# Kernel optimization log

Measured on AMD Instinct MI355X. Metric: run time of the kernel, lower is better.

The kernel has to match this reference:

```python
import jax, jax.numpy as jnp
import numpy as np

D_MODEL, D_HIDDEN, N_EXPERTS = 1024, 4096, 8
CAP_FACTOR, LBL_COEF, ZLOSS_COEF = 1.25, 0.01, 0.0


def setup_inputs() -> dict:
    key = jax.random.key(0)
    ks = jax.random.split(key, 4)
    B, T = 4, 2048
    x = jax.random.normal(ks[0], (B, T, D_MODEL), dtype=jnp.float32)
    # router linear
    Wr = jax.random.normal(ks[1], (D_MODEL, N_EXPERTS), jnp.float32) / np.sqrt(D_MODEL).astype(np.float32)
    br = jnp.zeros((N_EXPERTS,), jnp.float32)
    # per-expert MLP: fc1 [D->H], gelu, fc2 [H->D]
    W1 = jax.random.normal(ks[2], (N_EXPERTS, D_MODEL, D_HIDDEN), jnp.float32) / np.sqrt(D_MODEL).astype(np.float32)
    b1 = jnp.zeros((N_EXPERTS, D_HIDDEN), jnp.float32)
    W2 = jax.random.normal(ks[3], (N_EXPERTS, D_HIDDEN, D_MODEL), jnp.float32) / np.sqrt(D_HIDDEN).astype(np.float32)
    b2 = jnp.zeros((N_EXPERTS, D_MODEL), jnp.float32)
    return {"x": x, "Wr": Wr, "br": br, "W1": W1, "b1": b1, "W2": W2, "b2": b2}


def reference(x, Wr, br, W1, b1, W2, b2):
    B, T, D = x.shape
    N = B * T
    E = Wr.shape[1]
    cap = int(CAP_FACTOR * (N / E) + 1)  # static Python int

    h = x.reshape(N, D)
    # --- Top1Router ---
    logits = h @ Wr + br                              # [N, E]
    probs = jax.nn.softmax(logits, axis=-1)
    top1 = jnp.argmax(probs, axis=-1)                 # [N]
    w = jnp.take_along_axis(probs, top1[:, None], axis=1)  # [N, 1]
    assign = jax.nn.one_hot(top1, E, dtype=jnp.float32)    # constant wrt grads
    importance = probs.mean(axis=0)
    load = jax.lax.stop_gradient(assign).mean(axis=0)
    lb_loss = E * jnp.sum(importance * load)
    z_loss = jnp.mean(jax.nn.logsumexp(logits, axis=-1) ** 2)

    # --- capacity-based dispatch (first `cap` tokens per expert, token order) ---
    pos = (jnp.cumsum(assign, axis=0) * assign).sum(axis=-1).astype(jnp.int32) - 1  # [N] slot within expert
    keep = pos < cap
    slot = jnp.where(keep, pos, cap)  # dropped tokens -> overflow slot `cap`
    xe = jnp.zeros((E, cap + 1, D), x.dtype).at[top1, slot].set(h)[:, :cap]  # [E, cap, D]

    # --- per-expert MLP as grouped GEMMs ---
    he = jax.nn.gelu(jnp.einsum('ecd,edh->ech', xe, W1) + b1[:, None, :])    # [E, cap, H]
    ye = jnp.einsum('ech,ehd->ecd', he, W2) + b2[:, None, :]                 # [E, cap, D]

    # --- combine (gather back, scale by router weight, zero dropped) ---
    out = ye[top1, jnp.minimum(pos, cap - 1)] * w   # [N, D]
    out = jnp.where(keep[:, None], out, jnp.zeros((), x.dtype))
    y = out.reshape(B, T, D)
    aux = LBL_COEF * lb_loss + ZLOSS_COEF * z_loss
    return (y, aux)
```

## Files before the change

kernel.cpp:

```cpp
#include <hip/hip_runtime.h>
#include <hip/hip_bf16.h>

#define N_TOK 8192
#define DM    1024
#define DH    4096
#define NE    8
#define CAP   1281
#define CAPR  1408
#define ISTR  1536

typedef unsigned short u16;
typedef __attribute__((ext_vector_type(8))) __bf16 bf16x8;
typedef __attribute__((ext_vector_type(8))) short short8;
typedef __attribute__((ext_vector_type(4))) short s16x4;
typedef __attribute__((ext_vector_type(4))) float f4;

__device__ __forceinline__ u16 f2bf(float f){
  union { float f; unsigned u; } v; v.f = f;
  unsigned r = v.u + 0x7fffu + ((v.u >> 16) & 1u);
  return (u16)(r >> 16);
}

__device__ __forceinline__ float gelu_fast(float v){
  float u = 0.7978845608028654f * (v + 0.044715f * v * v * v);
  return v * __builtin_amdgcn_rcpf(1.0f + __expf(-2.0f * u));
}

__device__ __forceinline__ void gl2lds16(const void* g, void* l){
  __builtin_amdgcn_global_load_lds((const __attribute__((address_space(1))) void*)g,
                                   (__attribute__((address_space(3))) void*)l, 16, 0, 0);
}

__global__ __launch_bounds__(256) void tcvt_k(const float* __restrict__ in, u16* __restrict__ out,
                                              int K, int Nn){
  __shared__ float tile[64][68];
  size_t mb = (size_t)blockIdx.z * (size_t)K * (size_t)Nn;
  const float* ip = in + mb;
  u16* op = out + mb;
  int n0 = blockIdx.x*64, k0 = blockIdx.y*64;
  int t = threadIdx.x;
  int kr = t>>4, nc = (t&15)*4;
  #pragma unroll
  for (int ii=0;ii<4;ii++){
    f4 v = *(const f4*)&ip[(size_t)(k0+kr+16*ii)*Nn + n0 + nc];
    tile[kr+16*ii][nc+0] = v[0]; tile[kr+16*ii][nc+1] = v[1];
    tile[kr+16*ii][nc+2] = v[2]; tile[kr+16*ii][nc+3] = v[3];
  }
  __syncthreads();
  int nr = t>>2, kc = (t&3)*16;
  short8 o0, o1;
  #pragma unroll
  for (int c=0;c<8;c++){
    o0[c] = (short)f2bf(tile[kc+c][nr]);
    o1[c] = (short)f2bf(tile[kc+8+c][nr]);
  }
  *(short8*)&op[(size_t)(n0+nr)*K + k0 + kc] = o0;
  *(short8*)&op[(size_t)(n0+nr)*K + k0 + kc + 8] = o1;
}

__global__ __launch_bounds__(256) void router_k(const float* __restrict__ x, const float* __restrict__ Wr,
    const float* __restrict__ br, u16* __restrict__ Xb, int* __restrict__ top1,
    float* __restrict__ wgt, float* __restrict__ impSum){
  __shared__ float pSh[4][8];
  int wid = threadIdx.x >> 6, lane = threadIdx.x & 63;
  int n = blockIdx.x * 4 + wid;
  const float* xr = x + (size_t)n * DM;
  u16* xbr = Xb + (size_t)n * DM;
  float acc[8];
  #pragma unroll
  for (int e=0;e<8;e++) acc[e]=0.f;
  #pragma unroll
  for (int c=0;c<4;c++){
    int d0 = c*256 + lane*4;
    f4 xv = *(const f4*)(xr + d0);
    s16x4 xb;
    #pragma unroll
    for (int j=0;j<4;j++) xb[j] = (short)f2bf(xv[j]);
    *(s16x4*)(xbr + d0) = xb;
    #pragma unroll
    for (int j=0;j<4;j++){
      const float* wrow = Wr + (size_t)(d0+j)*NE;
      float xs = xv[j];
      #pragma unroll
      for (int e=0;e<8;e++) acc[e] = fmaf(xs, wrow[e], acc[e]);
    }
  }
  #pragma unroll
  for (int off=32; off>0; off>>=1){
    #pragma unroll
    for (int e=0;e<8;e++) acc[e] += __shfl_down(acc[e], off, 64);
  }
  if (lane==0){
    float lg[8]; float mx = -1e30f;
    #pragma unroll
    for (int e=0;e<8;e++){ lg[e] = acc[e] + br[e]; mx = fmaxf(mx, lg[e]); }
    float p[8], s=0.f;
    #pragma unroll
    for (int e=0;e<8;e++){ p[e] = expf(lg[e]-mx); s += p[e]; }
    int bt=0; float bv=lg[0];
    #pragma unroll
    for (int e=1;e<8;e++){ if (lg[e]>bv){ bv=lg[e]; bt=e; } }
    float inv = 1.f/s;
    top1[n] = bt; wgt[n] = p[bt]*inv;
    #pragma unroll
    for (int e=0;e<8;e++) pSh[wid][e] = p[e]*inv;
  }
  __syncthreads();
  if (threadIdx.x < 8){
    int e = threadIdx.x;
    atomicAdd(&impSum[e], pSh[0][e]+pSh[1][e]+pSh[2][e]+pSh[3][e]);
  }
}

__global__ __launch_bounds__(1024) void scan_k(const int* __restrict__ top1, int* __restrict__ idx,
    int* __restrict__ cnt, int* __restrict__ rawcnt, int* __restrict__ dropList,
    int* __restrict__ nDrop, const float* __restrict__ impSum, float* __restrict__ auxOut){
  __shared__ int waveCnt[16][8];
  __shared__ int wavePre[16][8];
  __shared__ int chunkTot[8];
  __shared__ int base_s[8];
  int tid = threadIdx.x, wid = tid>>6, lane = tid&63;
  if (tid < 8) base_s[tid] = 0;
  __syncthreads();
  for (int c=0;c<8;c++){
    int t = c*1024 + tid;
    int e = top1[t];
    int myPre = 0;
    #pragma unroll
    for (int ex=0; ex<8; ex++){
      unsigned long long mk = __ballot(e == ex);
      if (lane == 0) waveCnt[wid][ex] = __popcll(mk);
      if (ex == e) myPre = __popcll(mk & ((1ull<<lane)-1ull));
    }
    __syncthreads();
    if (tid < 8){
      int run = 0;
      for (int wv=0; wv<16; wv++){ wavePre[wv][tid] = run; run += waveCnt[wv][tid]; }
      chunkTot[tid] = run;
    }
    __syncthreads();
    int pos = base_s[e] + wavePre[wid][e] + myPre;
    if (pos < CAP) idx[e*ISTR + pos] = t;
    else { int d = atomicAdd(nDrop, 1); dropList[d] = t; }
    __syncthreads();
    if (tid < 8) base_s[tid] += chunkTot[tid];
    __syncthreads();
  }
  if (tid < 8){
    rawcnt[tid] = base_s[tid];
    cnt[tid] = base_s[tid] < CAP ? base_s[tid] : CAP;
  }
  if (tid == 0){
    float s = 0.f;
    for (int e=0;e<8;e++) s += (impSum[e]*(1.f/N_TOK)) * ((float)base_s[e]*(1.f/N_TOK));
    *auxOut = 0.01f * 8.f * s;
  }
}

__global__ __launch_bounds__(256) void zdrop_k(const int* __restrict__ dropList,
    const int* __restrict__ nDrop, float* __restrict__ y){
  int nd = *nDrop;
  for (int i = blockIdx.x; i < nd; i += gridDim.x){
    int t = dropList[i];
    f4* row = (f4*)(y + (size_t)t * DM);
    f4 z; z[0]=0.f; z[1]=0.f; z[2]=0.f; z[3]=0.f;
    row[threadIdx.x] = z;
  }
}


#define LDA(buf, m, kk) (*(const bf16x8*)&lds[(buf)*16384 + (aBase ^ ((kk)*32)) + (m)*1024])
#define LDB(buf, n, kk) (*(const bf16x8*)&lds[32768 + (buf)*16384 + (bBase ^ ((kk)*32)) + (n)*1024])

#define SA_J(buf, j, kc) gl2lds16(aS[j] + (size_t)(kc)*64, &lds[(buf)*16384 + ((j)*512 + t)*8])
#define SB_ALLM(buf, kc) do{ \
  gl2lds16(bS[0] + (size_t)(kc)*64, &lds[32768 + (buf)*16384 + (0*512 + t)*8]); \
  gl2lds16(bS[1] + (size_t)(kc)*64, &lds[32768 + (buf)*16384 + (1*512 + t)*8]); \
  gl2lds16(bS[2] + (size_t)(kc)*64, &lds[32768 + (buf)*16384 + (2*512 + t)*8]); \
  gl2lds16(bS[3] + (size_t)(kc)*64, &lds[32768 + (buf)*16384 + (3*512 + t)*8]); }while(0)

#define LGKM0 do{ asm volatile("s_waitcnt lgkmcnt(0)" ::: "memory"); \
                  __builtin_amdgcn_sched_barrier(0); }while(0)

#define MFMA_PAIR(q) \
  _Pragma("unroll") for (int j_=0;j_<2;j_++) \
    _Pragma("unroll") for (int n_=0;n_<4;n_++) \
      _Pragma("unroll") for (int kk_=0;kk_<2;kk_++) \
        acc[2*(q)+j_][n_] = __builtin_amdgcn_mfma_f32_16x16x32_bf16(a_[j_][kk_], Bf[n_][kk_], acc[2*(q)+j_][n_], 0,0,0);

#define KTILE(buf, ktv, NTv) do{ \
  int kc1 = (ktv)+1 < (NTv) ? (ktv)+1 : (NTv)-1; \
  int kc2 = (ktv)+2 < (NTv) ? (ktv)+2 : (NTv)-1; \
  bf16x8 a_[2][2]; \
   \
  asm volatile("s_waitcnt vmcnt(6)" ::: "memory"); \
  __builtin_amdgcn_s_barrier(); \
  _Pragma("unroll") for (int n_=0;n_<4;n_++){ Bf[n_][0] = LDB(buf,n_,0); Bf[n_][1] = LDB(buf,n_,1); } \
  a_[0][0]=LDA(buf,0,0); a_[0][1]=LDA(buf,0,1); a_[1][0]=LDA(buf,1,0); a_[1][1]=LDA(buf,1,1); \
  SA_J((buf)^1, 1, kc1); SA_J((buf)^1, 3, kc1); \
  LGKM0; \
  __builtin_amdgcn_s_setprio(1); MFMA_PAIR(0); __builtin_amdgcn_s_setprio(0); \
   \
  __builtin_amdgcn_s_barrier(); \
  a_[0][0]=LDA(buf,2,0); a_[0][1]=LDA(buf,2,1); a_[1][0]=LDA(buf,3,0); a_[1][1]=LDA(buf,3,1); \
  SB_ALLM(buf, kc2); \
  LGKM0; \
  __builtin_amdgcn_s_setprio(1); MFMA_PAIR(1); __builtin_amdgcn_s_setprio(0); \
   \
  __builtin_amdgcn_s_barrier(); \
  a_[0][0]=LDA(buf,4,0); a_[0][1]=LDA(buf,4,1); a_[1][0]=LDA(buf,5,0); a_[1][1]=LDA(buf,5,1); \
  SA_J(buf, 0, kc2); SA_J(buf, 2, kc2); \
  LGKM0; \
  __builtin_amdgcn_s_setprio(1); MFMA_PAIR(2); __builtin_amdgcn_s_setprio(0); \
   \
  __builtin_amdgcn_s_barrier(); \
  a_[0][0]=LDA(buf,6,0); a_[0][1]=LDA(buf,6,1); a_[1][0]=LDA(buf,7,0); a_[1][1]=LDA(buf,7,1); \
  LGKM0; \
  __builtin_amdgcn_s_setprio(1); MFMA_PAIR(3); __builtin_amdgcn_s_setprio(0); \
}while(0)

#define GEMM_PROLOGUE() do{ \
  SB_ALLM(0, 0); \
  SA_J(0,0,0); SA_J(0,2,0); \
  SA_J(0,1,0); SA_J(0,3,0); \
  SB_ALLM(1, 1); \
  SA_J(1,0,1); SA_J(1,2,1); }while(0)

__global__ __launch_bounds__(512, 2) void gemm1_k(
    const u16* __restrict__ Xb, const u16* __restrict__ W1T,
    const float* __restrict__ b1, const int* __restrict__ idx,
    const int* __restrict__ cnt, u16* __restrict__ He)
{
  int e = blockIdx.z, mt = blockIdx.y, nt = blockIdx.x;
  int cn = cnt[e];
  if (mt*256 >= cn) return;
  __shared__ __align__(16) u16 lds[65536];
  int t = threadIdx.x, lane = t&63, wid = t>>6;
  int waveM = wid>>2, waveN = wid&3;
  int rA = lane&15, kb = lane>>4, s = rA&7;

  const u16* aS[4]; const u16* bS[4];
  #pragma unroll
  for (int j=0;j<4;j++){
    int pos = j*512 + t;
    int row = pos>>3, ch = pos&7;
    int gcb = ch ^ (row&7);
    int slotrow = mt*256 + row;
    int token = (slotrow < cn) ? idx[e*ISTR + slotrow] : 0;
    aS[j] = Xb + (size_t)token*DM + gcb*8;
    bS[j] = W1T + ((size_t)e*DH + nt*256 + row)*DM + gcb*8;
  }
  f4 acc[8][4];
  #pragma unroll
  for (int m=0;m<8;m++)
    #pragma unroll
    for (int n=0;n<4;n++)
      #pragma unroll
      for (int j=0;j<4;j++) acc[m][n][j]=0.f;

  int aBase = (waveM*128 + rA)*64 + (kb ^ s)*8;
  int bBase = (waveN*64  + rA)*64 + (kb ^ s)*8;
  bf16x8 Bf[4][2];

  GEMM_PROLOGUE();
  const int NT = DM/64;
  #pragma unroll 1
  for (int i=0;i<NT/2;i++){
    KTILE(0, 2*i,   NT);
    KTILE(1, 2*i+1, NT);
  }
  asm volatile("s_waitcnt vmcnt(0) lgkmcnt(0)" ::: "memory");

  int rG = lane>>4;
  #pragma unroll
  for (int n=0;n<4;n++){
    int col = nt*256 + waveN*64 + n*16 + rA;
    float bias = b1[e*DH + col];
    #pragma unroll
    for (int m=0;m<8;m++){
      int slot = mt*256 + waveM*128 + m*16 + rG*4;
      if (slot < CAPR){
        u16* dst = He + ((size_t)e*CAPR + slot)*DH + col;
        #pragma unroll
        for (int j=0;j<4;j++){
          float v = acc[m][n][j] + bias;
          dst[(size_t)j*DH] = f2bf(gelu_fast(v));
        }
      }
    }
  }
}

__global__ __launch_bounds__(512, 2) void gemm2_k(
    const u16* __restrict__ He, const u16* __restrict__ W2T,
    const float* __restrict__ b2, const int* __restrict__ idx,
    const int* __restrict__ cnt, const float* __restrict__ wgt,
    float* __restrict__ y)
{
  int e = blockIdx.z, mt = blockIdx.y, nt = blockIdx.x;
  int cn = cnt[e];
  if (mt*256 >= cn) return;
  __shared__ __align__(16) u16 lds[65536];
  int t = threadIdx.x, lane = t&63, wid = t>>6;
  int waveM = wid>>2, waveN = wid&3;
  int rA = lane&15, kb = lane>>4, s = rA&7;

  const u16* aS[4]; const u16* bS[4];
  #pragma unroll
  for (int j=0;j<4;j++){
    int pos = j*512 + t;
    int row = pos>>3, ch = pos&7;
    int gcb = ch ^ (row&7);
    int srow = mt*256 + row; if (srow >= cn) srow = cn-1;
    aS[j] = He  + ((size_t)e*CAPR + srow)*DH + gcb*8;
    bS[j] = W2T + ((size_t)e*DM + nt*256 + row)*DH + gcb*8;
  }
  f4 acc[8][4];
  #pragma unroll
  for (int m=0;m<8;m++)
    #pragma unroll
    for (int n=0;n<4;n++)
      #pragma unroll
      for (int j=0;j<4;j++) acc[m][n][j]=0.f;

  int aBase = (waveM*128 + rA)*64 + (kb ^ s)*8;
  int bBase = (waveN*64  + rA)*64 + (kb ^ s)*8;
  bf16x8 Bf[4][2];

  GEMM_PROLOGUE();
  const int NT = DH/64;
  #pragma unroll 1
  for (int i=0;i<NT/2;i++){
    KTILE(0, 2*i,   NT);
    KTILE(1, 2*i+1, NT);
  }
  asm volatile("s_waitcnt vmcnt(0) lgkmcnt(0)" ::: "memory");

  int rG = lane>>4;
  float bias_[4];
  #pragma unroll
  for (int n=0;n<4;n++) bias_[n] = b2[e*DM + nt*256 + waveN*64 + n*16 + rA];
  #pragma unroll
  for (int m=0;m<8;m++){
    int slot0 = mt*256 + waveM*128 + m*16 + rG*4;
    #pragma unroll
    for (int j=0;j<4;j++){
      int slot = slot0 + j;
      bool valid = slot < cn;
      int tk = valid ? idx[e*ISTR + slot] : 0;
      float wv = valid ? wgt[tk] : 0.f;
      float* yr = y + (size_t)tk*DM;
      #pragma unroll
      for (int n=0;n<4;n++){
        int col = nt*256 + waveN*64 + n*16 + rA;
        if (valid) yr[col] = (acc[m][n][j] + bias_[n]) * wv;
      }
    }
  }
}

extern "C" void kernel_launch(void* const* d_in, const int* in_sizes, int n_in,
                              void* d_out, int out_size, void* d_ws, size_t ws_size,
                              hipStream_t stream){
  const float* x  = (const float*)d_in[0];
  const float* Wr = (const float*)d_in[1];
  const float* br = (const float*)d_in[2];
  const float* W1 = (const float*)d_in[3];
  const float* b1 = (const float*)d_in[4];
  const float* W2 = (const float*)d_in[5];
  const float* b2 = (const float*)d_in[6];
  float* y = (float*)d_out;

  char* ws = (char*)d_ws;
  u16* Xb  = (u16*)(ws);
  u16* W1T = (u16*)(ws + 16777216ull);
  u16* W2T = (u16*)(ws + 16777216ull + 67108864ull);
  u16* He  = (u16*)(ws + 16777216ull + 2ull*67108864ull);
  char* tail = ws + 16777216ull + 2ull*67108864ull + (size_t)NE*CAPR*DH*2ull;
  int*   top1 = (int*)(tail);
  float* wgt  = (float*)(tail + 32768);
  int*   idx  = (int*)(tail + 65536);
  int*   drop = (int*)(tail + 65536 + 49152);
  float* impSum = (float*)(tail + 65536 + 49152 + 32768);
  int*   nDrop  = (int*)((char*)impSum + 32);
  int*   cnt    = nDrop + 1;
  int*   rawcnt = cnt + 8;

  (void)hipMemsetAsync(impSum, 0, 64, stream);

  tcvt_k<<<dim3(64,16,8), 256, 0, stream>>>(W1, W1T, DM, DH);
  tcvt_k<<<dim3(16,64,8), 256, 0, stream>>>(W2, W2T, DH, DM);
  router_k<<<2048, 256, 0, stream>>>(x, Wr, br, Xb, top1, wgt, impSum);
  scan_k<<<1, 1024, 0, stream>>>(top1, idx, cnt, rawcnt, drop, nDrop, impSum,
                                 y + (size_t)N_TOK*DM);
  zdrop_k<<<64, 256, 0, stream>>>(drop, nDrop, y);
  gemm1_k<<<dim3(DH/256, 6, NE), 512, 0, stream>>>(Xb, W1T, b1, idx, cnt, He);
  gemm2_k<<<dim3(DM/256, 6, NE), 512, 0, stream>>>(He, W2T, b2, idx, cnt, wgt, y);

  (void)in_sizes; (void)n_in; (void)out_size; (void)ws_size;
}
```

Baseline: 356.2 us.

## Split-K the second expert GEMM, stage epilogues through LDS, add combine kernel

Splits the second expert GEMM's K dimension in two, so each half writes fp32 partial sums to a workspace buffer and the launch gets more blocks to fill the device. A new per-token combine kernel adds the two partials and the bias, applies the router weight and zeroes dropped tokens, replacing the drop-list zeroing kernel and the scattered epilogue writes. Both GEMM epilogues now stage tiles in LDS so global stores are coalesced vector writes. The first GEMM grid is cut to 5 row tiles and partials are sized for 1280 slots, so a token landing in slot 1280 (capacity 1281) would not be computed correctly. The change also adds extra traffic for the partial buffer.

```diff
diff --git a/kernel.cpp b/kernel.cpp
--- a/kernel.cpp
+++ b/kernel.cpp
@@ -8,6 +8,7 @@
 #define CAP   1281
 #define CAPR  1408
 #define ISTR  1536
+#define PR    1280
 
 typedef unsigned short u16;
 typedef __attribute__((ext_vector_type(8))) __bf16 bf16x8;
@@ -113,8 +114,8 @@
 }
 
 __global__ __launch_bounds__(1024) void scan_k(const int* __restrict__ top1, int* __restrict__ idx,
-    int* __restrict__ cnt, int* __restrict__ rawcnt, int* __restrict__ dropList,
-    int* __restrict__ nDrop, const float* __restrict__ impSum, float* __restrict__ auxOut){
+    int* __restrict__ slotOf, int* __restrict__ cnt,
+    const float* __restrict__ impSum, float* __restrict__ auxOut){
   __shared__ int waveCnt[16][8];
   __shared__ int wavePre[16][8];
   __shared__ int chunkTot[8];
@@ -140,14 +141,14 @@
     }
     __syncthreads();
     int pos = base_s[e] + wavePre[wid][e] + myPre;
-    if (pos < CAP) idx[e*ISTR + pos] = t;
-    else { int d = atomicAdd(nDrop, 1); dropList[d] = t; }
+    bool keep = pos < CAP;
+    if (keep) idx[e*ISTR + pos] = t;
+    slotOf[t] = keep ? pos : -1;
     __syncthreads();
     if (tid < 8) base_s[tid] += chunkTot[tid];
     __syncthreads();
   }
   if (tid < 8){
-    rawcnt[tid] = base_s[tid];
     cnt[tid] = base_s[tid] < CAP ? base_s[tid] : CAP;
   }
   if (tid == 0){
@@ -157,15 +158,25 @@
   }
 }
 
-__global__ __launch_bounds__(256) void zdrop_k(const int* __restrict__ dropList,
-    const int* __restrict__ nDrop, float* __restrict__ y){
-  int nd = *nDrop;
-  for (int i = blockIdx.x; i < nd; i += gridDim.x){
-    int t = dropList[i];
-    f4* row = (f4*)(y + (size_t)t * DM);
-    f4 z; z[0]=0.f; z[1]=0.f; z[2]=0.f; z[3]=0.f;
-    row[threadIdx.x] = z;
-  }
+__global__ __launch_bounds__(256) void combine_k(const float* __restrict__ part,
+    const float* __restrict__ b2, const int* __restrict__ top1,
+    const int* __restrict__ slotOf, const float* __restrict__ wgt,
+    float* __restrict__ y){
+  int t = blockIdx.x;
+  int d = threadIdx.x*4;
+  int s = slotOf[t];
+  f4 o; o[0]=0.f; o[1]=0.f; o[2]=0.f; o[3]=0.f;
+  if (s >= 0){
+    int e = top1[t];
+    float w = wgt[t];
+    size_t base = ((size_t)e*PR + s)*DM + d;
+    f4 a = *(const f4*)&part[base];
+    f4 b = *(const f4*)&part[(size_t)NE*PR*DM + base];
+    f4 c = *(const f4*)&b2[e*DM + d];
+    #pragma unroll
+    for (int i=0;i<4;i++) o[i] = (a[i]+b[i]+c[i])*w;
+  }
+  *(f4*)&y[(size_t)t*DM + d] = o;
 }
 
 
@@ -192,7 +203,6 @@
   int kc1 = (ktv)+1 < (NTv) ? (ktv)+1 : (NTv)-1; \
   int kc2 = (ktv)+2 < (NTv) ? (ktv)+2 : (NTv)-1; \
   bf16x8 a_[2][2]; \
-   \
   asm volatile("s_waitcnt vmcnt(6)" ::: "memory"); \
   __builtin_amdgcn_s_barrier(); \
   _Pragma("unroll") for (int n_=0;n_<4;n_++){ Bf[n_][0] = LDB(buf,n_,0); Bf[n_][1] = LDB(buf,n_,1); } \
@@ -200,19 +210,16 @@
   SA_J((buf)^1, 1, kc1); SA_J((buf)^1, 3, kc1); \
   LGKM0; \
   __builtin_amdgcn_s_setprio(1); MFMA_PAIR(0); __builtin_amdgcn_s_setprio(0); \
-   \
   __builtin_amdgcn_s_barrier(); \
   a_[0][0]=LDA(buf,2,0); a_[0][1]=LDA(buf,2,1); a_[1][0]=LDA(buf,3,0); a_[1][1]=LDA(buf,3,1); \
   SB_ALLM(buf, kc2); \
   LGKM0; \
   __builtin_amdgcn_s_setprio(1); MFMA_PAIR(1); __builtin_amdgcn_s_setprio(0); \
-   \
   __builtin_amdgcn_s_barrier(); \
   a_[0][0]=LDA(buf,4,0); a_[0][1]=LDA(buf,4,1); a_[1][0]=LDA(buf,5,0); a_[1][1]=LDA(buf,5,1); \
   SA_J(buf, 0, kc2); SA_J(buf, 2, kc2); \
   LGKM0; \
   __builtin_amdgcn_s_setprio(1); MFMA_PAIR(2); __builtin_amdgcn_s_setprio(0); \
-   \
   __builtin_amdgcn_s_barrier(); \
   a_[0][0]=LDA(buf,6,0); a_[0][1]=LDA(buf,6,1); a_[1][0]=LDA(buf,7,0); a_[1][1]=LDA(buf,7,1); \
   LGKM0; \
@@ -270,34 +277,40 @@
     KTILE(1, 2*i+1, NT);
   }
   asm volatile("s_waitcnt vmcnt(0) lgkmcnt(0)" ::: "memory");
+  __builtin_amdgcn_s_barrier();
 
   int rG = lane>>4;
-  #pragma unroll
-  for (int n=0;n<4;n++){
-    int col = nt*256 + waveN*64 + n*16 + rA;
-    float bias = b1[e*DH + col];
-    #pragma unroll
-    for (int m=0;m<8;m++){
-      int slot = mt*256 + waveM*128 + m*16 + rG*4;
-      if (slot < CAPR){
-        u16* dst = He + ((size_t)e*CAPR + slot)*DH + col;
-        #pragma unroll
-        for (int j=0;j<4;j++){
-          float v = acc[m][n][j] + bias;
-          dst[(size_t)j*DH] = f2bf(gelu_fast(v));
-        }
-      }
+  float bias_[4];
+  #pragma unroll
+  for (int n=0;n<4;n++) bias_[n] = b1[e*DH + nt*256 + waveN*64 + n*16 + rA];
+  u16* stg = &lds[wid*1280];
+  #pragma unroll 1
+  for (int m=0;m<8;m++){
+    #pragma unroll
+    for (int n=0;n<4;n++)
+      #pragma unroll
+      for (int j=0;j<4;j++)
+        stg[(rG*4+j)*72 + n*16 + rA] = f2bf(gelu_fast(acc[m][n][j] + bias_[n]));
+    asm volatile("s_waitcnt lgkmcnt(0)" ::: "memory");
+    __builtin_amdgcn_sched_barrier(0);
+    int slot = mt*256 + waveM*128 + m*16;
+    #pragma unroll
+    for (int h=0;h<2;h++){
+      int row16 = h*8 + (lane>>3);
+      int c8 = (lane&7)*8;
+      bf16x8 v = *(const bf16x8*)&stg[row16*72 + c8];
+      *(bf16x8*)&He[((size_t)e*CAPR + slot + row16)*DH + nt*256 + waveN*64 + c8] = v;
     }
+    asm volatile("s_waitcnt lgkmcnt(0)" ::: "memory");
+    __builtin_amdgcn_sched_barrier(0);
   }
 }
 
 __global__ __launch_bounds__(512, 2) void gemm2_k(
     const u16* __restrict__ He, const u16* __restrict__ W2T,
-    const float* __restrict__ b2, const int* __restrict__ idx,
-    const int* __restrict__ cnt, const float* __restrict__ wgt,
-    float* __restrict__ y)
+    const int* __restrict__ cnt, float* __restrict__ part)
 {
-  int e = blockIdx.z, mt = blockIdx.y, nt = blockIdx.x;
+  int e = blockIdx.z, mt = blockIdx.y >> 1, ks = blockIdx.y & 1, nt = blockIdx.x;
   int cn = cnt[e];
   if (mt*256 >= cn) return;
   __shared__ __align__(16) u16 lds[65536];
@@ -312,8 +325,8 @@
     int row = pos>>3, ch = pos&7;
     int gcb = ch ^ (row&7);
     int srow = mt*256 + row; if (srow >= cn) srow = cn-1;
-    aS[j] = He  + ((size_t)e*CAPR + srow)*DH + gcb*8;
-    bS[j] = W2T + ((size_t)e*DM + nt*256 + row)*DH + gcb*8;
+    aS[j] = He  + ((size_t)e*CAPR + srow)*DH + ks*2048 + gcb*8;
+    bS[j] = W2T + ((size_t)e*DM + nt*256 + row)*DH + ks*2048 + gcb*8;
   }
   f4 acc[8][4];
   #pragma unroll
@@ -328,34 +341,37 @@
   bf16x8 Bf[4][2];
 
   GEMM_PROLOGUE();
-  const int NT = DH/64;
+  const int NT = 2048/64;
   #pragma unroll 1
   for (int i=0;i<NT/2;i++){
     KTILE(0, 2*i,   NT);
     KTILE(1, 2*i+1, NT);
   }
   asm volatile("s_waitcnt vmcnt(0) lgkmcnt(0)" ::: "memory");
+  __builtin_amdgcn_s_barrier();
 
   int rG = lane>>4;
-  float bias_[4];
-  #pragma unroll
-  for (int n=0;n<4;n++) bias_[n] = b2[e*DM + nt*256 + waveN*64 + n*16 + rA];
-  #pragma unroll
+  float* stgf = ((float*)lds) + wid*1088;
+  float* pOut = part + ((size_t)ks*NE + e)*((size_t)PR*DM);
+  #pragma unroll 1
   for (int m=0;m<8;m++){
-    int slot0 = mt*256 + waveM*128 + m*16 + rG*4;
-    #pragma unroll
-    for (int j=0;j<4;j++){
-      int slot = slot0 + j;
-      bool valid = slot < cn;
-      int tk = valid ? idx[e*ISTR + slot] : 0;
-      float wv = valid ? wgt[tk] : 0.f;
-      float* yr = y + (size_t)tk*DM;
+    #pragma unroll
+    for (int n=0;n<4;n++)
       #pragma unroll
-      for (int n=0;n<4;n++){
-        int col = nt*256 + waveN*64 + n*16 + rA;
-        if (valid) yr[col] = (acc[m][n][j] + bias_[n]) * wv;
-      }
+      for (int j=0;j<4;j++)
+        stgf[(rG*4+j)*68 + n*16 + rA] = acc[m][n][j];
+    asm volatile("s_waitcnt lgkmcnt(0)" ::: "memory");
+    __builtin_amdgcn_sched_barrier(0);
+    int slot = mt*256 + waveM*128 + m*16;
+    #pragma unroll
+    for (int it=0; it<4; it++){
+      int row16 = it*4 + rG;
+      int wc = (lane&15)*4;
+      f4 v = *(const f4*)&stgf[row16*68 + wc];
+      *(f4*)&pOut[(size_t)(slot+row16)*DM + nt*256 + waveN*64 + wc] = v;
     }
+    asm volatile("s_waitcnt lgkmcnt(0)" ::: "memory");
+    __builtin_amdgcn_sched_barrier(0);
   }
 }
 
@@ -374,28 +390,26 @@
   char* ws = (char*)d_ws;
   u16* Xb  = (u16*)(ws);
   u16* W1T = (u16*)(ws + 16777216ull);
-  u16* W2T = (u16*)(ws + 16777216ull + 67108864ull);
-  u16* He  = (u16*)(ws + 16777216ull + 2ull*67108864ull);
-  char* tail = ws + 16777216ull + 2ull*67108864ull + (size_t)NE*CAPR*DH*2ull;
-  int*   top1 = (int*)(tail);
-  float* wgt  = (float*)(tail + 32768);
-  int*   idx  = (int*)(tail + 65536);
-  int*   drop = (int*)(tail + 65536 + 49152);
+  float* part = (float*)ws;
+  u16* W2T = (u16*)(ws + 83886080ull);
+  u16* He  = (u16*)(ws + 83886080ull + 67108864ull);
+  char* tail = ws + 83886080ull + 67108864ull + (size_t)NE*CAPR*DH*2ull;
+  int*   top1   = (int*)(tail);
+  float* wgt    = (float*)(tail + 32768);
+  int*   idx    = (int*)(tail + 65536);
+  int*   slotOf = (int*)(tail + 65536 + 49152);
   float* impSum = (float*)(tail + 65536 + 49152 + 32768);
-  int*   nDrop  = (int*)((char*)impSum + 32);
-  int*   cnt    = nDrop + 1;
-  int*   rawcnt = cnt + 8;
-
-  (void)hipMemsetAsync(impSum, 0, 64, stream);
+  int*   cnt    = (int*)((char*)impSum + 32);
+
+  (void)hipMemsetAsync(impSum, 0, 32, stream);
 
   tcvt_k<<<dim3(64,16,8), 256, 0, stream>>>(W1, W1T, DM, DH);
   tcvt_k<<<dim3(16,64,8), 256, 0, stream>>>(W2, W2T, DH, DM);
   router_k<<<2048, 256, 0, stream>>>(x, Wr, br, Xb, top1, wgt, impSum);
-  scan_k<<<1, 1024, 0, stream>>>(top1, idx, cnt, rawcnt, drop, nDrop, impSum,
-                                 y + (size_t)N_TOK*DM);
-  zdrop_k<<<64, 256, 0, stream>>>(drop, nDrop, y);
-  gemm1_k<<<dim3(DH/256, 6, NE), 512, 0, stream>>>(Xb, W1T, b1, idx, cnt, He);
-  gemm2_k<<<dim3(DM/256, 6, NE), 512, 0, stream>>>(He, W2T, b2, idx, cnt, wgt, y);
+  scan_k<<<1, 1024, 0, stream>>>(top1, idx, slotOf, cnt, impSum, y + (size_t)N_TOK*DM);
+  gemm1_k<<<dim3(DH/256, 5, NE), 512, 0, stream>>>(Xb, W1T, b1, idx, cnt, He);
+  gemm2_k<<<dim3(DM/256, 10, NE), 512, 0, stream>>>(He, W2T, cnt, part);
+  combine_k<<<N_TOK, 256, 0, stream>>>(part, b2, top1, slotOf, wgt, y);
 
   (void)in_sizes; (void)n_in; (void)out_size; (void)ws_size;
 }
```

New measurement: 476.6 us. +33.8%, slower.

## Fuse fp32-to-bf16 weight conversion into GEMM B-tile loads, drop transpose kernels

Applied to the files above, without the earlier changes.

Removes the two separate transpose-and-convert passes over W1 and W2. Each GEMM now reads fp32 weight rows straight into registers, packs them to bf16 with v_cvt_pk_bf16_f32 and writes them into swizzled LDS, using a new LDB addressing scheme and a reworked prefetch and waitcnt schedule. It also flattens the grid and maps blocks so that tiles sharing an expert and N-tile stay on the same XCD. The cost is twice the global weight bytes per GEMM tile, re-read by every M-tile, plus extra VALU conversion work inside the main loop.

```diff
diff --git a/kernel.cpp b/kernel.cpp
--- a/kernel.cpp
+++ b/kernel.cpp
@@ -14,6 +14,7 @@
 typedef __attribute__((ext_vector_type(8))) short short8;
 typedef __attribute__((ext_vector_type(4))) short s16x4;
 typedef __attribute__((ext_vector_type(4))) float f4;
+typedef __attribute__((ext_vector_type(4))) unsigned int ui32x4;
 
 __device__ __forceinline__ u16 f2bf(float f){
   union { float f; unsigned u; } v; v.f = f;
@@ -29,33 +30,6 @@
 __device__ __forceinline__ void gl2lds16(const void* g, void* l){
   __builtin_amdgcn_global_load_lds((const __attribute__((address_space(1))) void*)g,
                                    (__attribute__((address_space(3))) void*)l, 16, 0, 0);
-}
-
-__global__ __launch_bounds__(256) void tcvt_k(const float* __restrict__ in, u16* __restrict__ out,
-                                              int K, int Nn){
-  __shared__ float tile[64][68];
-  size_t mb = (size_t)blockIdx.z * (size_t)K * (size_t)Nn;
-  const float* ip = in + mb;
-  u16* op = out + mb;
-  int n0 = blockIdx.x*64, k0 = blockIdx.y*64;
-  int t = threadIdx.x;
-  int kr = t>>4, nc = (t&15)*4;
-  #pragma unroll
-  for (int ii=0;ii<4;ii++){
-    f4 v = *(const f4*)&ip[(size_t)(k0+kr+16*ii)*Nn + n0 + nc];
-    tile[kr+16*ii][nc+0] = v[0]; tile[kr+16*ii][nc+1] = v[1];
-    tile[kr+16*ii][nc+2] = v[2]; tile[kr+16*ii][nc+3] = v[3];
-  }
-  __syncthreads();
-  int nr = t>>2, kc = (t&3)*16;
-  short8 o0, o1;
-  #pragma unroll
-  for (int c=0;c<8;c++){
-    o0[c] = (short)f2bf(tile[kc+c][nr]);
-    o1[c] = (short)f2bf(tile[kc+8+c][nr]);
-  }
-  *(short8*)&op[(size_t)(n0+nr)*K + k0 + kc] = o0;
-  *(short8*)&op[(size_t)(n0+nr)*K + k0 + kc + 8] = o1;
 }
 
 __global__ __launch_bounds__(256) void router_k(const float* __restrict__ x, const float* __restrict__ Wr,
@@ -113,8 +87,8 @@
 }
 
 __global__ __launch_bounds__(1024) void scan_k(const int* __restrict__ top1, int* __restrict__ idx,
-    int* __restrict__ cnt, int* __restrict__ rawcnt, int* __restrict__ dropList,
-    int* __restrict__ nDrop, const float* __restrict__ impSum, float* __restrict__ auxOut){
+    int* __restrict__ cnt, int* __restrict__ dropList, int* __restrict__ nDrop,
+    const float* __restrict__ impSum, float* __restrict__ auxOut){
   __shared__ int waveCnt[16][8];
   __shared__ int wavePre[16][8];
   __shared__ int chunkTot[8];
@@ -147,7 +121,6 @@
     __syncthreads();
   }
   if (tid < 8){
-    rawcnt[tid] = base_s[tid];
     cnt[tid] = base_s[tid] < CAP ? base_s[tid] : CAP;
   }
   if (tid == 0){
@@ -170,14 +143,29 @@
 
 
 #define LDA(buf, m, kk) (*(const bf16x8*)&lds[(buf)*16384 + (aBase ^ ((kk)*32)) + (m)*1024])
-#define LDB(buf, n, kk) (*(const bf16x8*)&lds[32768 + (buf)*16384 + (bBase ^ ((kk)*32)) + (n)*1024])
-
-#define SA_J(buf, j, kc) gl2lds16(aS[j] + (size_t)(kc)*64, &lds[(buf)*16384 + ((j)*512 + t)*8])
-#define SB_ALLM(buf, kc) do{ \
-  gl2lds16(bS[0] + (size_t)(kc)*64, &lds[32768 + (buf)*16384 + (0*512 + t)*8]); \
-  gl2lds16(bS[1] + (size_t)(kc)*64, &lds[32768 + (buf)*16384 + (1*512 + t)*8]); \
-  gl2lds16(bS[2] + (size_t)(kc)*64, &lds[32768 + (buf)*16384 + (2*512 + t)*8]); \
-  gl2lds16(bS[3] + (size_t)(kc)*64, &lds[32768 + (buf)*16384 + (3*512 + t)*8]); }while(0)
+#define LDB(buf, n_, kk) (*(const bf16x8*)&lds[32768 + (buf)*16384 + \
+  (waveN*64 + (n_)*16 + rA)*64 + ((((kb ^ ((4*(n_) + (rA>>2)) & 7)))*8) ^ ((kk)*32))])
+
+#define SA_ALL(buf, kc) do{ \
+  gl2lds16(aS[0] + (size_t)(kc)*64, &lds[(buf)*16384 + (0*512 + t)*8]); \
+  gl2lds16(aS[1] + (size_t)(kc)*64, &lds[(buf)*16384 + (1*512 + t)*8]); \
+  gl2lds16(aS[2] + (size_t)(kc)*64, &lds[(buf)*16384 + (2*512 + t)*8]); \
+  gl2lds16(aS[3] + (size_t)(kc)*64, &lds[(buf)*16384 + (3*512 + t)*8]); }while(0)
+
+#define BLOAD(kc) do{ \
+  const float* _r = wB + (size_t)((kc)*64 + wid*8)*NW + (lane<<2); \
+  _Pragma("unroll") for (int j_=0;j_<8;j_++) br[j_] = *(const f4*)(_r + (size_t)j_*NW); }while(0)
+
+#define CVTW_B(bufsel) do{ \
+  _Pragma("unroll") for (int i_=0;i_<4;i_++){ \
+    unsigned _q0,_q1,_q2,_q3; \
+    asm volatile("v_cvt_pk_bf16_f32 %0, %1, %2" : "=v"(_q0) : "v"(br[0][i_]), "v"(br[1][i_])); \
+    asm volatile("v_cvt_pk_bf16_f32 %0, %1, %2" : "=v"(_q1) : "v"(br[2][i_]), "v"(br[3][i_])); \
+    asm volatile("v_cvt_pk_bf16_f32 %0, %1, %2" : "=v"(_q2) : "v"(br[4][i_]), "v"(br[5][i_])); \
+    asm volatile("v_cvt_pk_bf16_f32 %0, %1, %2" : "=v"(_q3) : "v"(br[6][i_]), "v"(br[7][i_])); \
+    ui32x4 _qq; _qq[0]=_q0; _qq[1]=_q1; _qq[2]=_q2; _qq[3]=_q3; \
+    *(ui32x4*)&lds[32768 + (bufsel)*16384 + 256*lane + 64*i_ + 8*(wid ^ (lane&7))] = _qq; \
+  } }while(0)
 
 #define LGKM0 do{ asm volatile("s_waitcnt lgkmcnt(0)" ::: "memory"); \
                   __builtin_amdgcn_sched_barrier(0); }while(0)
@@ -193,45 +181,51 @@
   int kc2 = (ktv)+2 < (NTv) ? (ktv)+2 : (NTv)-1; \
   bf16x8 a_[2][2]; \
    \
-  asm volatile("s_waitcnt vmcnt(6)" ::: "memory"); \
+  asm volatile("s_waitcnt vmcnt(8)" ::: "memory"); \
   __builtin_amdgcn_s_barrier(); \
   _Pragma("unroll") for (int n_=0;n_<4;n_++){ Bf[n_][0] = LDB(buf,n_,0); Bf[n_][1] = LDB(buf,n_,1); } \
   a_[0][0]=LDA(buf,0,0); a_[0][1]=LDA(buf,0,1); a_[1][0]=LDA(buf,1,0); a_[1][1]=LDA(buf,1,1); \
-  SA_J((buf)^1, 1, kc1); SA_J((buf)^1, 3, kc1); \
+  SA_ALL((buf)^1, kc1); \
   LGKM0; \
   __builtin_amdgcn_s_setprio(1); MFMA_PAIR(0); __builtin_amdgcn_s_setprio(0); \
    \
   __builtin_amdgcn_s_barrier(); \
   a_[0][0]=LDA(buf,2,0); a_[0][1]=LDA(buf,2,1); a_[1][0]=LDA(buf,3,0); a_[1][1]=LDA(buf,3,1); \
-  SB_ALLM(buf, kc2); \
   LGKM0; \
   __builtin_amdgcn_s_setprio(1); MFMA_PAIR(1); __builtin_amdgcn_s_setprio(0); \
    \
   __builtin_amdgcn_s_barrier(); \
   a_[0][0]=LDA(buf,4,0); a_[0][1]=LDA(buf,4,1); a_[1][0]=LDA(buf,5,0); a_[1][1]=LDA(buf,5,1); \
-  SA_J(buf, 0, kc2); SA_J(buf, 2, kc2); \
   LGKM0; \
   __builtin_amdgcn_s_setprio(1); MFMA_PAIR(2); __builtin_amdgcn_s_setprio(0); \
    \
   __builtin_amdgcn_s_barrier(); \
   a_[0][0]=LDA(buf,6,0); a_[0][1]=LDA(buf,6,1); a_[1][0]=LDA(buf,7,0); a_[1][1]=LDA(buf,7,1); \
+  asm volatile("s_waitcnt vmcnt(4)" ::: "memory"); \
+  CVTW_B((buf)^1); \
+  BLOAD(kc2); \
   LGKM0; \
   __builtin_amdgcn_s_setprio(1); MFMA_PAIR(3); __builtin_amdgcn_s_setprio(0); \
 }while(0)
 
 #define GEMM_PROLOGUE() do{ \
-  SB_ALLM(0, 0); \
-  SA_J(0,0,0); SA_J(0,2,0); \
-  SA_J(0,1,0); SA_J(0,3,0); \
-  SB_ALLM(1, 1); \
-  SA_J(1,0,1); SA_J(1,2,1); }while(0)
+  BLOAD(0); \
+  SA_ALL(0, 0); \
+  asm volatile("s_waitcnt vmcnt(4)" ::: "memory"); \
+  CVTW_B(0); \
+  BLOAD(1); \
+  LGKM0; }while(0)
 
 __global__ __launch_bounds__(512, 2) void gemm1_k(
-    const u16* __restrict__ Xb, const u16* __restrict__ W1T,
+    const u16* __restrict__ Xb, const float* __restrict__ W1,
     const float* __restrict__ b1, const int* __restrict__ idx,
     const int* __restrict__ cnt, u16* __restrict__ He)
 {
-  int e = blockIdx.z, mt = blockIdx.y, nt = blockIdx.x;
+  int bid = blockIdx.x;
+  int xcd = bid & 7, q = bid >> 3;
+  int gi = q / 6, mt = q - gi*6;
+  int g = gi*8 + xcd;
+  int e = g >> 4, nt = g & 15;
   int cn = cnt[e];
   if (mt*256 >= cn) return;
   __shared__ __align__(16) u16 lds[65536];
@@ -239,7 +233,7 @@
   int waveM = wid>>2, waveN = wid&3;
   int rA = lane&15, kb = lane>>4, s = rA&7;
 
-  const u16* aS[4]; const u16* bS[4];
+  const u16* aS[4];
   #pragma unroll
   for (int j=0;j<4;j++){
     int pos = j*512 + t;
@@ -248,8 +242,10 @@
     int slotrow = mt*256 + row;
     int token = (slotrow < cn) ? idx[e*ISTR + slotrow] : 0;
     aS[j] = Xb + (size_t)token*DM + gcb*8;
-    bS[j] = W1T + ((size_t)e*DH + nt*256 + row)*DM + gcb*8;
-  }
+  }
+  const float* wB = W1 + (size_t)e*DM*DH + nt*256;
+  const int NW = DH;
+  f4 br[8];
   f4 acc[8][4];
   #pragma unroll
   for (int m=0;m<8;m++)
@@ -259,7 +255,6 @@
       for (int j=0;j<4;j++) acc[m][n][j]=0.f;
 
   int aBase = (waveM*128 + rA)*64 + (kb ^ s)*8;
-  int bBase = (waveN*64  + rA)*64 + (kb ^ s)*8;
   bf16x8 Bf[4][2];
 
   GEMM_PROLOGUE();
@@ -292,12 +287,16 @@
 }
 
 __global__ __launch_bounds__(512, 2) void gemm2_k(
-    const u16* __restrict__ He, const u16* __restrict__ W2T,
+    const u16* __restrict__ He, const float* __restrict__ W2,
     const float* __restrict__ b2, const int* __restrict__ idx,
     const int* __restrict__ cnt, const float* __restrict__ wgt,
     float* __restrict__ y)
 {
-  int e = blockIdx.z, mt = blockIdx.y, nt = blockIdx.x;
+  int bid = blockIdx.x;
+  int xcd = bid & 7, q = bid >> 3;
+  int gi = q / 6, mt = q - gi*6;
+  int g = gi*8 + xcd;
+  int e = g >> 2, nt = g & 3;
   int cn = cnt[e];
   if (mt*256 >= cn) return;
   __shared__ __align__(16) u16 lds[65536];
@@ -305,16 +304,18 @@
   int waveM = wid>>2, waveN = wid&3;
   int rA = lane&15, kb = lane>>4, s = rA&7;
 
-  const u16* aS[4]; const u16* bS[4];
+  const u16* aS[4];
   #pragma unroll
   for (int j=0;j<4;j++){
     int pos = j*512 + t;
     int row = pos>>3, ch = pos&7;
     int gcb = ch ^ (row&7);
     int srow = mt*256 + row; if (srow >= cn) srow = cn-1;
-    aS[j] = He  + ((size_t)e*CAPR + srow)*DH + gcb*8;
-    bS[j] = W2T + ((size_t)e*DM + nt*256 + row)*DH + gcb*8;
-  }
+    aS[j] = He + ((size_t)e*CAPR + srow)*DH + gcb*8;
+  }
+  const float* wB = W2 + (size_t)e*DH*DM + nt*256;
+  const int NW = DM;
+  f4 br[8];
   f4 acc[8][4];
   #pragma unroll
   for (int m=0;m<8;m++)
@@ -324,7 +325,6 @@
       for (int j=0;j<4;j++) acc[m][n][j]=0.f;
 
   int aBase = (waveM*128 + rA)*64 + (kb ^ s)*8;
-  int bBase = (waveN*64  + rA)*64 + (kb ^ s)*8;
   bf16x8 Bf[4][2];
 
   GEMM_PROLOGUE();
@@ -373,29 +373,24 @@
 
   char* ws = (char*)d_ws;
   u16* Xb  = (u16*)(ws);
-  u16* W1T = (u16*)(ws + 16777216ull);
-  u16* W2T = (u16*)(ws + 16777216ull + 67108864ull);
-  u16* He  = (u16*)(ws + 16777216ull + 2ull*67108864ull);
-  char* tail = ws + 16777216ull + 2ull*67108864ull + (size_t)NE*CAPR*DH*2ull;
-  int*   top1 = (int*)(tail);
-  float* wgt  = (float*)(tail + 32768);
-  int*   idx  = (int*)(tail + 65536);
-  int*   drop = (int*)(tail + 65536 + 49152);
+  u16* He  = (u16*)(ws + 16777216ull);
+  char* tail = ws + 16777216ull + (size_t)NE*CAPR*DH*2ull;
+  int*   top1   = (int*)(tail);
+  float* wgt    = (float*)(tail + 32768);
+  int*   idx    = (int*)(tail + 65536);
+  int*   drop   = (int*)(tail + 65536 + 49152);
   float* impSum = (float*)(tail + 65536 + 49152 + 32768);
   int*   nDrop  = (int*)((char*)impSum + 32);
   int*   cnt    = nDrop + 1;
-  int*   rawcnt = cnt + 8;
 
   (void)hipMemsetAsync(impSum, 0, 64, stream);
 
-  tcvt_k<<<dim3(64,16,8), 256, 0, stream>>>(W1, W1T, DM, DH);
-  tcvt_k<<<dim3(16,64,8), 256, 0, stream>>>(W2, W2T, DH, DM);
   router_k<<<2048, 256, 0, stream>>>(x, Wr, br, Xb, top1, wgt, impSum);
-  scan_k<<<1, 1024, 0, stream>>>(top1, idx, cnt, rawcnt, drop, nDrop, impSum,
+  scan_k<<<1, 1024, 0, stream>>>(top1, idx, cnt, drop, nDrop, impSum,
                                  y + (size_t)N_TOK*DM);
   zdrop_k<<<64, 256, 0, stream>>>(drop, nDrop, y);
-  gemm1_k<<<dim3(DH/256, 6, NE), 512, 0, stream>>>(Xb, W1T, b1, idx, cnt, He);
-  gemm2_k<<<dim3(DM/256, 6, NE), 512, 0, stream>>>(He, W2T, b2, idx, cnt, wgt, y);
+  gemm1_k<<<768, 512, 0, stream>>>(Xb, W1, b1, idx, cnt, He);
+  gemm2_k<<<192, 512, 0, stream>>>(He, W2, b2, idx, cnt, wgt, y);
 
   (void)in_sizes; (void)n_in; (void)out_size; (void)ws_size;
 }
```

Result: slower. 425.8 us (+19.6%).

## Swap GEMM1 operand roles, vectorize He stores, and remap blocks for XCD locality

Applied to the files above, without the earlier changes.

GEMM1 now treats W1T as the M operand and gathered tokens as the N operand, so the accumulator layout lets each lane write four contiguous bf16 hidden values with a single 8-byte store. The bias is loaded as a float4. Both GEMMs switch to a 1D grid with a block-index remap that groups tiles of the same expert and weight slice onto the same XCD, aiming for better L2 reuse. The rawcnt output is removed. One risk is that the He padding rows between cn and CAPR are no longer written, although GEMM2 clamps its reads to cn-1.

```diff
diff --git a/kernel.cpp b/kernel.cpp
--- a/kernel.cpp
+++ b/kernel.cpp
@@ -113,8 +113,8 @@
 }
 
 __global__ __launch_bounds__(1024) void scan_k(const int* __restrict__ top1, int* __restrict__ idx,
-    int* __restrict__ cnt, int* __restrict__ rawcnt, int* __restrict__ dropList,
-    int* __restrict__ nDrop, const float* __restrict__ impSum, float* __restrict__ auxOut){
+    int* __restrict__ cnt, int* __restrict__ dropList, int* __restrict__ nDrop,
+    const float* __restrict__ impSum, float* __restrict__ auxOut){
   __shared__ int waveCnt[16][8];
   __shared__ int wavePre[16][8];
   __shared__ int chunkTot[8];
@@ -147,7 +147,6 @@
     __syncthreads();
   }
   if (tid < 8){
-    rawcnt[tid] = base_s[tid];
     cnt[tid] = base_s[tid] < CAP ? base_s[tid] : CAP;
   }
   if (tid == 0){
@@ -168,7 +167,6 @@
   }
 }
 
-
 #define LDA(buf, m, kk) (*(const bf16x8*)&lds[(buf)*16384 + (aBase ^ ((kk)*32)) + (m)*1024])
 #define LDB(buf, n, kk) (*(const bf16x8*)&lds[32768 + (buf)*16384 + (bBase ^ ((kk)*32)) + (n)*1024])
 
@@ -192,7 +190,6 @@
   int kc1 = (ktv)+1 < (NTv) ? (ktv)+1 : (NTv)-1; \
   int kc2 = (ktv)+2 < (NTv) ? (ktv)+2 : (NTv)-1; \
   bf16x8 a_[2][2]; \
-   \
   asm volatile("s_waitcnt vmcnt(6)" ::: "memory"); \
   __builtin_amdgcn_s_barrier(); \
   _Pragma("unroll") for (int n_=0;n_<4;n_++){ Bf[n_][0] = LDB(buf,n_,0); Bf[n_][1] = LDB(buf,n_,1); } \
@@ -200,19 +197,16 @@
   SA_J((buf)^1, 1, kc1); SA_J((buf)^1, 3, kc1); \
   LGKM0; \
   __builtin_amdgcn_s_setprio(1); MFMA_PAIR(0); __builtin_amdgcn_s_setprio(0); \
-   \
   __builtin_amdgcn_s_barrier(); \
   a_[0][0]=LDA(buf,2,0); a_[0][1]=LDA(buf,2,1); a_[1][0]=LDA(buf,3,0); a_[1][1]=LDA(buf,3,1); \
   SB_ALLM(buf, kc2); \
   LGKM0; \
   __builtin_amdgcn_s_setprio(1); MFMA_PAIR(1); __builtin_amdgcn_s_setprio(0); \
-   \
   __builtin_amdgcn_s_barrier(); \
   a_[0][0]=LDA(buf,4,0); a_[0][1]=LDA(buf,4,1); a_[1][0]=LDA(buf,5,0); a_[1][1]=LDA(buf,5,1); \
   SA_J(buf, 0, kc2); SA_J(buf, 2, kc2); \
   LGKM0; \
   __builtin_amdgcn_s_setprio(1); MFMA_PAIR(2); __builtin_amdgcn_s_setprio(0); \
-   \
   __builtin_amdgcn_s_barrier(); \
   a_[0][0]=LDA(buf,6,0); a_[0][1]=LDA(buf,6,1); a_[1][0]=LDA(buf,7,0); a_[1][1]=LDA(buf,7,1); \
   LGKM0; \
@@ -231,9 +225,13 @@
     const float* __restrict__ b1, const int* __restrict__ idx,
     const int* __restrict__ cnt, u16* __restrict__ He)
 {
-  int e = blockIdx.z, mt = blockIdx.y, nt = blockIdx.x;
+  int bid = blockIdx.x;
+  int x = bid & 7, k = bid >> 3;
+  int g = x*16 + k/6;
+  int ntS = k - (k/6)*6;
+  int e = g >> 4, mtH = g & 15;
   int cn = cnt[e];
-  if (mt*256 >= cn) return;
+  if (ntS*256 >= cn) return;
   __shared__ __align__(16) u16 lds[65536];
   int t = threadIdx.x, lane = t&63, wid = t>>6;
   int waveM = wid>>2, waveN = wid&3;
@@ -245,10 +243,10 @@
     int pos = j*512 + t;
     int row = pos>>3, ch = pos&7;
     int gcb = ch ^ (row&7);
-    int slotrow = mt*256 + row;
+    aS[j] = W1T + ((size_t)e*DH + mtH*256 + row)*DM + gcb*8;
+    int slotrow = ntS*256 + row;
     int token = (slotrow < cn) ? idx[e*ISTR + slotrow] : 0;
-    aS[j] = Xb + (size_t)token*DM + gcb*8;
-    bS[j] = W1T + ((size_t)e*DH + nt*256 + row)*DM + gcb*8;
+    bS[j] = Xb + (size_t)token*DM + gcb*8;
   }
   f4 acc[8][4];
   #pragma unroll
@@ -273,19 +271,17 @@
 
   int rG = lane>>4;
   #pragma unroll
-  for (int n=0;n<4;n++){
-    int col = nt*256 + waveN*64 + n*16 + rA;
-    float bias = b1[e*DH + col];
-    #pragma unroll
-    for (int m=0;m<8;m++){
-      int slot = mt*256 + waveM*128 + m*16 + rG*4;
-      if (slot < CAPR){
-        u16* dst = He + ((size_t)e*CAPR + slot)*DH + col;
+  for (int m=0;m<8;m++){
+    int h0 = mtH*256 + waveM*128 + m*16 + rG*4;
+    f4 b4 = *(const f4*)&b1[e*DH + h0];
+    #pragma unroll
+    for (int n=0;n<4;n++){
+      int slot = ntS*256 + waveN*64 + n*16 + rA;
+      if (slot < cn){
+        s16x4 v;
         #pragma unroll
-        for (int j=0;j<4;j++){
-          float v = acc[m][n][j] + bias;
-          dst[(size_t)j*DH] = f2bf(gelu_fast(v));
-        }
+        for (int j=0;j<4;j++) v[j] = (short)f2bf(gelu_fast(acc[m][n][j] + b4[j]));
+        *(s16x4*)&He[((size_t)e*CAPR + slot)*DH + h0] = v;
       }
     }
   }
@@ -297,7 +293,11 @@
     const int* __restrict__ cnt, const float* __restrict__ wgt,
     float* __restrict__ y)
 {
-  int e = blockIdx.z, mt = blockIdx.y, nt = blockIdx.x;
+  int bid = blockIdx.x;
+  int x = bid & 7, k = bid >> 3;
+  int g = x*4 + k/6;
+  int mt = k - (k/6)*6;
+  int e = g >> 2, nt = g & 3;
   int cn = cnt[e];
   if (mt*256 >= cn) return;
   __shared__ __align__(16) u16 lds[65536];
@@ -377,25 +377,24 @@
   u16* W2T = (u16*)(ws + 16777216ull + 67108864ull);
   u16* He  = (u16*)(ws + 16777216ull + 2ull*67108864ull);
   char* tail = ws + 16777216ull + 2ull*67108864ull + (size_t)NE*CAPR*DH*2ull;
-  int*   top1 = (int*)(tail);
-  float* wgt  = (float*)(tail + 32768);
-  int*   idx  = (int*)(tail + 65536);
-  int*   drop = (int*)(tail + 65536 + 49152);
+  int*   top1   = (int*)(tail);
+  float* wgt    = (float*)(tail + 32768);
+  int*   idx    = (int*)(tail + 65536);
+  int*   drop   = (int*)(tail + 65536 + 49152);
   float* impSum = (float*)(tail + 65536 + 49152 + 32768);
   int*   nDrop  = (int*)((char*)impSum + 32);
   int*   cnt    = nDrop + 1;
-  int*   rawcnt = cnt + 8;
 
   (void)hipMemsetAsync(impSum, 0, 64, stream);
 
   tcvt_k<<<dim3(64,16,8), 256, 0, stream>>>(W1, W1T, DM, DH);
   tcvt_k<<<dim3(16,64,8), 256, 0, stream>>>(W2, W2T, DH, DM);
   router_k<<<2048, 256, 0, stream>>>(x, Wr, br, Xb, top1, wgt, impSum);
-  scan_k<<<1, 1024, 0, stream>>>(top1, idx, cnt, rawcnt, drop, nDrop, impSum,
+  scan_k<<<1, 1024, 0, stream>>>(top1, idx, cnt, drop, nDrop, impSum,
                                  y + (size_t)N_TOK*DM);
   zdrop_k<<<64, 256, 0, stream>>>(drop, nDrop, y);
-  gemm1_k<<<dim3(DH/256, 6, NE), 512, 0, stream>>>(Xb, W1T, b1, idx, cnt, He);
-  gemm2_k<<<dim3(DM/256, 6, NE), 512, 0, stream>>>(He, W2T, b2, idx, cnt, wgt, y);
+  gemm1_k<<<768, 512, 0, stream>>>(Xb, W1T, b1, idx, cnt, He);
+  gemm2_k<<<192, 512, 0, stream>>>(He, W2T, b2, idx, cnt, wgt, y);
 
   (void)in_sizes; (void)n_in; (void)out_size; (void)ws_size;
 }
```

Measured after the change: 348.4 us. -2.2%, faster.
